# Performance work log

Hardware: AMD Instinct MI355X
Metric: run time of the kernel (lower is better)

## Reference

```python
import jax, jax.numpy as jnp
import numpy as np

# (l, C_l, C_l_TP, C_l_angular) per non-empty l-block of the filter type
FILTER_REPS = [(0, 144, 144, 1), (1, 272, 272, 1), (2, 208, 208, 1), (3, 80, 80, 1), (4, 16, 16, 1)]
FILTER_C = 720      # sum of C_l
FILTER_DIM = 2704   # sum of C_l*(2l+1)
ANG_DIM = 25        # sum of C_l_angular*(2l+1)
DIM_OUT = 52
DIM_IN = 52
Q_OUT, Q_IN, NUM_P = 16, 16, 125
SCALAR_BASIS = 12


def setup_inputs() -> dict:
    key = jax.random.key(0)
    k1, k2, k3, k4, k5 = jax.random.split(key, 5)
    N = Q_OUT * Q_IN * NUM_P
    scalar_kernel_tensor = jax.random.normal(k1, (Q_OUT, Q_IN, NUM_P, SCALAR_BASIS), dtype=jnp.float32)
    angular_kernel_tensor = jax.random.normal(k2, (N, ANG_DIM), dtype=jnp.float32)
    weights = jax.random.normal(k3, (SCALAR_BASIS, FILTER_C), dtype=jnp.float32)
    # TP mixing matrix is a constant sparse buffer (Wigner-3j based); model as sparsified dense
    dense = jax.random.normal(k4, (DIM_OUT * DIM_IN, FILTER_DIM), dtype=jnp.float32)
    mask = jax.random.uniform(k5, (DIM_OUT * DIM_IN, FILTER_DIM)) < 0.05
    TP_mixing = dense * mask.astype(jnp.float32)
    return {"scalar_kernel_tensor": scalar_kernel_tensor,
            "angular_kernel_tensor": angular_kernel_tensor,
            "weights": weights,
            "TP_mixing": TP_mixing}


def mul_scalar_angular(sc, ang):
    # sc: (N, FILTER_C), ang: (N, ANG_DIM) -> (N, FILTER_DIM)
    N = sc.shape[0]
    outs = []
    s = 0
    a = 0
    for (l, C_l, C_l_TP, C_l_ang) in FILTER_REPS:
        m = 2 * l + 1
        dim_ang = C_l_ang * m
        x = (sc[:, s:s + C_l].reshape(N, C_l_ang, C_l_TP, 1)
             * ang[:, a:a + dim_ang].reshape(N, C_l_ang, 1, m))
        outs.append(x.reshape(N, C_l * m))
        s += C_l
        a += dim_ang
    return jnp.concatenate(outs, axis=-1)


def reference(scalar_kernel_tensor, angular_kernel_tensor, weights, TP_mixing):
    N = Q_OUT * Q_IN * NUM_P
    sk = scalar_kernel_tensor.reshape(N, SCALAR_BASIS)
    # combine scalar basis with weights: (N, FILTER_C)
    sc = jnp.einsum('ns,sc->nc', sk, weights / jnp.sqrt(jnp.float32(SCALAR_BASIS)))
    # ragged segment-wise broadcast multiply: (N, FILTER_DIM)
    filt = mul_scalar_angular(sc, angular_kernel_tensor)
    # kernel = (TP_mixing @ filt.T).T == filt @ TP_mixing.T : (N, DIM_OUT*DIM_IN)
    k = filt @ TP_mixing.T
    return k.reshape(Q_OUT, Q_IN, NUM_P, DIM_OUT, DIM_IN)
```

## Files before the change

kernel.cpp:

```cpp
#include <hip/hip_runtime.h>
#include <hip/hip_bf16.h>

#define N_ROWS 32000
#define SB     12
#define FC     720
#define FD     2704
#define OCOLS  2704
#define OPAD   2816
#define ANGD   25
#define PDIM   300
#define KST    320
#define NT     5

typedef __attribute__((ext_vector_type(8))) short bf16x8;
typedef __attribute__((ext_vector_type(4))) float f32x4;

__device__ __forceinline__ void gload16(const void* g, void* l) {
    __builtin_amdgcn_global_load_lds(
        (const __attribute__((address_space(1))) void*)g,
        (__attribute__((address_space(3))) void*)l, 16, 0, 0);
}

__global__ __launch_bounds__(320) void build_V(
    const float* __restrict__ TP,
    const float* __restrict__ W,
    __hip_bfloat16* __restrict__ V)
{
    const int o   = blockIdx.x;
    const int tid = threadIdx.x;
    __shared__ float s_tp[FD];
    __shared__ float s_w[SB * FC];

    const float inv = 0.28867513459481288f;
    for (int i = tid; i < SB * FC; i += 320) s_w[i] = W[i] * inv;
    if (o < OCOLS) {
        for (int i = tid; i < FD; i += 320) s_tp[i] = TP[(size_t)o * FD + i];
    } else {
        for (int i = tid; i < FD; i += 320) s_tp[i] = 0.f;
    }
    __syncthreads();

    const int p = tid;
    float acc = 0.f;
    if (p < PDIM) {
        const int s     = p / ANGD;
        const int alpha = p - s * ANGD;
        int m, off, sco, al, Cl;
        if (alpha < 1)       { m = 1; off = 0;    sco = 0;   al = 0;  Cl = 144; }
        else if (alpha < 4)  { m = 3; off = 144;  sco = 144; al = 1;  Cl = 272; }
        else if (alpha < 9)  { m = 5; off = 960;  sco = 416; al = 4;  Cl = 208; }
        else if (alpha < 16) { m = 7; off = 2000; sco = 624; al = 9;  Cl = 80;  }
        else                 { m = 9; off = 2560; sco = 704; al = 16; Cl = 16;  }
        const int j = alpha - al;
        const float* tp = s_tp + off + j;
        const float* ww = s_w + s * FC + sco;
        float a0 = 0.f, a1 = 0.f, a2 = 0.f, a3 = 0.f;
        for (int c = 0; c < Cl; c += 4) {
            a0 += tp[(c + 0) * m] * ww[c + 0];
            a1 += tp[(c + 1) * m] * ww[c + 1];
            a2 += tp[(c + 2) * m] * ww[c + 2];
            a3 += tp[(c + 3) * m] * ww[c + 3];
        }
        acc = (a0 + a1) + (a2 + a3);
    }
    if (p < KST) V[(size_t)o * KST + p] = __float2bfloat16(acc);
}

__global__ void build_X(const float* __restrict__ sk,
                        const float* __restrict__ ang,
                        __hip_bfloat16* __restrict__ X)
{
    const int idx = blockIdx.x * 256 + threadIdx.x;
    if (idx >= N_ROWS * (KST / 8)) return;
    const int n  = idx / (KST / 8);
    const int p0 = (idx - n * (KST / 8)) * 8;
    const float* skn  = sk  + (size_t)n * SB;
    const float* angn = ang + (size_t)n * ANGD;
    alignas(16) __hip_bfloat16 tmp[8];
    #pragma unroll
    for (int u = 0; u < 8; ++u) {
        const int p = p0 + u;
        float v = 0.f;
        if (p < PDIM) {
            const int s = p / ANGD;
            const int a = p - s * ANGD;
            v = skn[s] * angn[a];
        }
        tmp[u] = __float2bfloat16(v);
    }
    *(bf16x8*)(X + (size_t)n * KST + p0) = *(const bf16x8*)tmp;
}

__global__ __launch_bounds__(512, 4) void gemm_bt(
    const __hip_bfloat16* __restrict__ A,
    const __hip_bfloat16* __restrict__ B,
    float* __restrict__ C)
{
    __shared__ __align__(1024) char lds[65536];
    char* const bufA = lds;
    char* const bufB = lds + 32768;
    float* const s_c = (float*)lds;

    const int tid  = threadIdx.x;
    const int wave = tid >> 6;
    const int lane = tid & 63;

    const int bn = blockIdx.x;
    const int bm = blockIdx.y;
    const size_t arow0 = (size_t)bm * 128;
    const size_t brow0 = (size_t)bn * 128;

    const int wr = wave >> 2;
    const int wc = wave & 3;

    const int lrow  = lane >> 3;
    const int lslot = ((lane & 7) ^ (lrow & 7)) << 4;

    auto STAGE = [&](const char* gbase, size_t growbase, int t, char* lbase) {
        const char* g0 = gbase + (growbase + (size_t)(wave * 8 + lrow)) * (KST * 2)
                               + (size_t)t * 128 + lslot;
        gload16(g0,                          lbase + wave * 1024);
        gload16(g0 + (size_t)64 * (KST * 2), lbase + 8192 + wave * 1024);
    };

    const int rl   = lane & 15;
    const int koct = lane >> 4;
    const int sK0 = ((0 * 4 + koct) ^ (lane & 7)) << 4;
    const int sK1 = ((1 * 4 + koct) ^ (lane & 7)) << 4;

    STAGE((const char*)A, arow0, 0, bufA + 0);
    STAGE((const char*)B, brow0, 0, bufB + 0);
    STAGE((const char*)A, arow0, 1, bufA + 16384);
    STAGE((const char*)B, brow0, 1, bufB + 16384);
    asm volatile("s_waitcnt vmcnt(4)" ::: "memory");
    __builtin_amdgcn_s_barrier();

    f32x4 acc[4][2] = {};

    for (int t = 0; t < NT; ++t) {
        char* const aC = bufA + (t & 1) * 16384;
        char* const bC = bufB + (t & 1) * 16384;

        bf16x8 af[4][2], bfr[2][2];
        #pragma unroll
        for (int m = 0; m < 4; ++m) {
            const int r = wr * 64 + m * 16 + rl;
            af[m][0] = *(const bf16x8*)(aC + r * 128 + sK0);
            af[m][1] = *(const bf16x8*)(aC + r * 128 + sK1);
        }
        #pragma unroll
        for (int n = 0; n < 2; ++n) {
            const int r = wc * 32 + n * 16 + rl;
            bfr[n][0] = *(const bf16x8*)(bC + r * 128 + sK0);
            bfr[n][1] = *(const bf16x8*)(bC + r * 128 + sK1);
        }
        asm volatile("s_waitcnt lgkmcnt(0)" ::: "memory");
        __builtin_amdgcn_sched_barrier(0);
        __builtin_amdgcn_s_barrier();

        if (t + 2 < NT) {
            STAGE((const char*)A, arow0, t + 2, aC);
            STAGE((const char*)B, brow0, t + 2, bC);
        }

        __builtin_amdgcn_s_setprio(1);
        #pragma unroll
        for (int ks = 0; ks < 2; ++ks)
            #pragma unroll
            for (int m = 0; m < 4; ++m)
                #pragma unroll
                for (int n = 0; n < 2; ++n)
                    acc[m][n] = __builtin_amdgcn_mfma_f32_16x16x32_bf16(
                        bfr[n][ks], af[m][ks], acc[m][n], 0, 0, 0);
        __builtin_amdgcn_s_setprio(0);
        __builtin_amdgcn_sched_barrier(0);

        if (t < NT - 2)       asm volatile("s_waitcnt vmcnt(4)" ::: "memory");
        else if (t == NT - 2) asm volatile("s_waitcnt vmcnt(0)" ::: "memory");
        if (t < NT - 1) __builtin_amdgcn_s_barrier();
    }

    #pragma unroll
    for (int h = 0; h < 2; ++h) {
        __syncthreads();
        if (wr == h) {
            #pragma unroll
            for (int m = 0; m < 4; ++m) {
                const int row_l = m * 16 + rl;
                #pragma unroll
                for (int n = 0; n < 2; ++n) {
                    const int col = wc * 32 + n * 16 + koct * 4;
                    *(f32x4*)&s_c[row_l * 132 + col] = acc[m][n];
                }
            }
        }
        __syncthreads();
        #pragma unroll
        for (int rr = 0; rr < 4; ++rr) {
            const int idx  = rr * 512 + tid;
            const int row  = idx >> 5;
            const int g4   = (idx & 31) * 4;
            if ((int)brow0 + g4 < OCOLS) {
                const f32x4 v = *(const f32x4*)&s_c[row * 132 + g4];
                __builtin_nontemporal_store(v,
                    (f32x4*)(C + (size_t)(arow0 + h * 64 + row) * OCOLS + brow0 + g4));
            }
        }
    }
}

extern "C" void kernel_launch(void* const* d_in, const int* in_sizes, int n_in,
                              void* d_out, int out_size, void* d_ws, size_t ws_size,
                              hipStream_t stream)
{
    const float* sk  = (const float*)d_in[0];
    const float* ang = (const float*)d_in[1];
    const float* W   = (const float*)d_in[2];
    const float* TP  = (const float*)d_in[3];
    float* out = (float*)d_out;

    __hip_bfloat16* X  = (__hip_bfloat16*)d_ws;
    __hip_bfloat16* Vb = X + (size_t)N_ROWS * KST;

    build_V<<<OPAD, 320, 0, stream>>>(TP, W, Vb);
    build_X<<<(N_ROWS * (KST / 8) + 255) / 256, 256, 0, stream>>>(sk, ang, X);

    dim3 grid(OPAD / 128, N_ROWS / 128);
    gemm_bt<<<grid, 512, 0, stream>>>(X, Vb, out);
}
```

Before: 156.9 us.

## Load GEMM B operand straight to registers and merge the two prep kernels

The GEMM no longer stages the B tile (V) through LDS. Each wave loads its B fragments directly from global memory into double-buffered registers one k-step ahead, while A keeps its LDS double buffer. This cuts LDS per block from 64KB to about 34KB, which can allow more resident blocks per CU, and it reorganises the vmcnt waits around the new load order. The separate build_V and build_X launches are also merged into one prep kernel, keyed on block index, to save a launch. The risk is redundant global reads of B across waves and more register pressure.

```diff
diff --git a/kernel.cpp b/kernel.cpp
--- a/kernel.cpp
+++ b/kernel.cpp
@@ -21,74 +21,74 @@
         (__attribute__((address_space(3))) void*)l, 16, 0, 0);
 }
 
-__global__ __launch_bounds__(320) void build_V(
+__global__ __launch_bounds__(320) void prep(
     const float* __restrict__ TP,
     const float* __restrict__ W,
-    __hip_bfloat16* __restrict__ V)
+    const float* __restrict__ sk,
+    const float* __restrict__ ang,
+    __hip_bfloat16* __restrict__ V,
+    __hip_bfloat16* __restrict__ X)
 {
-    const int o   = blockIdx.x;
     const int tid = threadIdx.x;
-    __shared__ float s_tp[FD];
-    __shared__ float s_w[SB * FC];
-
-    const float inv = 0.28867513459481288f;
-    for (int i = tid; i < SB * FC; i += 320) s_w[i] = W[i] * inv;
-    if (o < OCOLS) {
-        for (int i = tid; i < FD; i += 320) s_tp[i] = TP[(size_t)o * FD + i];
+    if (blockIdx.x < OPAD) {
+        const int o = blockIdx.x;
+        __shared__ float s_tp[FD];
+        __shared__ float s_w[SB * FC];
+
+        const float inv = 0.28867513459481288f;
+        for (int i = tid; i < SB * FC; i += 320) s_w[i] = W[i] * inv;
+        if (o < OCOLS) {
+            for (int i = tid; i < FD; i += 320) s_tp[i] = TP[(size_t)o * FD + i];
+        } else {
+            for (int i = tid; i < FD; i += 320) s_tp[i] = 0.f;
+        }
+        __syncthreads();
+
+        const int p = tid;
+        float acc = 0.f;
+        if (p < PDIM) {
+            const int s     = p / ANGD;
+            const int alpha = p - s * ANGD;
+            int m, off, sco, al, Cl;
+            if (alpha < 1)       { m = 1; off = 0;    sco = 0;   al = 0;  Cl = 144; }
+            else if (alpha < 4)  { m = 3; off = 144;  sco = 144; al = 1;  Cl = 272; }
+            else if (alpha < 9)  { m = 5; off = 960;  sco = 416; al = 4;  Cl = 208; }
+            else if (alpha < 16) { m = 7; off = 2000; sco = 624; al = 9;  Cl = 80;  }
+            else                 { m = 9; off = 2560; sco = 704; al = 16; Cl = 16;  }
+            const int j = alpha - al;
+            const float* tp = s_tp + off + j;
+            const float* ww = s_w + s * FC + sco;
+            float a0 = 0.f, a1 = 0.f, a2 = 0.f, a3 = 0.f;
+            for (int c = 0; c < Cl; c += 4) {
+                a0 += tp[(c + 0) * m] * ww[c + 0];
+                a1 += tp[(c + 1) * m] * ww[c + 1];
+                a2 += tp[(c + 2) * m] * ww[c + 2];
+                a3 += tp[(c + 3) * m] * ww[c + 3];
+            }
+            acc = (a0 + a1) + (a2 + a3);
+        }
+        if (p < KST) V[(size_t)o * KST + p] = __float2bfloat16(acc);
     } else {
-        for (int i = tid; i < FD; i += 320) s_tp[i] = 0.f;
+        const int idx = (blockIdx.x - OPAD) * 320 + tid;
+        if (idx >= N_ROWS * (KST / 8)) return;
+        const int n  = idx / (KST / 8);
+        const int p0 = (idx - n * (KST / 8)) * 8;
+        const float* skn  = sk  + (size_t)n * SB;
+        const float* angn = ang + (size_t)n * ANGD;
+        alignas(16) __hip_bfloat16 tmp[8];
+        #pragma unroll
+        for (int u = 0; u < 8; ++u) {
+            const int p = p0 + u;
+            float v = 0.f;
+            if (p < PDIM) {
+                const int s = p / ANGD;
+                const int a = p - s * ANGD;
+                v = skn[s] * angn[a];
+            }
+            tmp[u] = __float2bfloat16(v);
+        }
+        *(bf16x8*)(X + (size_t)n * KST + p0) = *(const bf16x8*)tmp;
     }
-    __syncthreads();
-
-    const int p = tid;
-    float acc = 0.f;
-    if (p < PDIM) {
-        const int s     = p / ANGD;
-        const int alpha = p - s * ANGD;
-        int m, off, sco, al, Cl;
-        if (alpha < 1)       { m = 1; off = 0;    sco = 0;   al = 0;  Cl = 144; }
-        else if (alpha < 4)  { m = 3; off = 144;  sco = 144; al = 1;  Cl = 272; }
-        else if (alpha < 9)  { m = 5; off = 960;  sco = 416; al = 4;  Cl = 208; }
-        else if (alpha < 16) { m = 7; off = 2000; sco = 624; al = 9;  Cl = 80;  }
-        else                 { m = 9; off = 2560; sco = 704; al = 16; Cl = 16;  }
-        const int j = alpha - al;
-        const float* tp = s_tp + off + j;
-        const float* ww = s_w + s * FC + sco;
-        float a0 = 0.f, a1 = 0.f, a2 = 0.f, a3 = 0.f;
-        for (int c = 0; c < Cl; c += 4) {
-            a0 += tp[(c + 0) * m] * ww[c + 0];
-            a1 += tp[(c + 1) * m] * ww[c + 1];
-            a2 += tp[(c + 2) * m] * ww[c + 2];
-            a3 += tp[(c + 3) * m] * ww[c + 3];
-        }
-        acc = (a0 + a1) + (a2 + a3);
-    }
-    if (p < KST) V[(size_t)o * KST + p] = __float2bfloat16(acc);
-}
-
-__global__ void build_X(const float* __restrict__ sk,
-                        const float* __restrict__ ang,
-                        __hip_bfloat16* __restrict__ X)
-{
-    const int idx = blockIdx.x * 256 + threadIdx.x;
-    if (idx >= N_ROWS * (KST / 8)) return;
-    const int n  = idx / (KST / 8);
-    const int p0 = (idx - n * (KST / 8)) * 8;
-    const float* skn  = sk  + (size_t)n * SB;
-    const float* angn = ang + (size_t)n * ANGD;
-    alignas(16) __hip_bfloat16 tmp[8];
-    #pragma unroll
-    for (int u = 0; u < 8; ++u) {
-        const int p = p0 + u;
-        float v = 0.f;
-        if (p < PDIM) {
-            const int s = p / ANGD;
-            const int a = p - s * ANGD;
-            v = skn[s] * angn[a];
-        }
-        tmp[u] = __float2bfloat16(v);
-    }
-    *(bf16x8*)(X + (size_t)n * KST + p0) = *(const bf16x8*)tmp;
 }
 
 __global__ __launch_bounds__(512, 4) void gemm_bt(
@@ -96,9 +96,8 @@
     const __hip_bfloat16* __restrict__ B,
     float* __restrict__ C)
 {
-    __shared__ __align__(1024) char lds[65536];
+    __shared__ __align__(1024) char lds[34816];
     char* const bufA = lds;
-    char* const bufB = lds + 32768;
     float* const s_c = (float*)lds;
 
     const int tid  = threadIdx.x;
@@ -115,10 +114,10 @@
 
     const int lrow  = lane >> 3;
     const int lslot = ((lane & 7) ^ (lrow & 7)) << 4;
-
-    auto STAGE = [&](const char* gbase, size_t growbase, int t, char* lbase) {
-        const char* g0 = gbase + (growbase + (size_t)(wave * 8 + lrow)) * (KST * 2)
-                               + (size_t)t * 128 + lslot;
+    auto STAGE_A = [&](int t, char* lbase) {
+        const char* g0 = (const char*)A
+            + (arow0 + (size_t)(wave * 8 + lrow)) * (KST * 2)
+            + (size_t)t * 128 + lslot;
         gload16(g0,                          lbase + wave * 1024);
         gload16(g0 + (size_t)64 * (KST * 2), lbase + 8192 + wave * 1024);
     };
@@ -128,40 +127,44 @@
     const int sK0 = ((0 * 4 + koct) ^ (lane & 7)) << 4;
     const int sK1 = ((1 * 4 + koct) ^ (lane & 7)) << 4;
 
-    STAGE((const char*)A, arow0, 0, bufA + 0);
-    STAGE((const char*)B, brow0, 0, bufB + 0);
-    STAGE((const char*)A, arow0, 1, bufA + 16384);
-    STAGE((const char*)B, brow0, 1, bufB + 16384);
-    asm volatile("s_waitcnt vmcnt(4)" ::: "memory");
+    const char* const Bb = (const char*)B;
+    const size_t boff0 = (brow0 + (size_t)(wc * 32 + 0 * 16 + rl)) * (KST * 2) + koct * 16;
+    const size_t boff1 = (brow0 + (size_t)(wc * 32 + 1 * 16 + rl)) * (KST * 2) + koct * 16;
+
+    bf16x8 bfr[2][2][2];
+    auto LOADB = [&](int t, int slot) {
+        bfr[slot][0][0] = *(const bf16x8*)(Bb + boff0 + t * 128 + 0);
+        bfr[slot][0][1] = *(const bf16x8*)(Bb + boff0 + t * 128 + 64);
+        bfr[slot][1][0] = *(const bf16x8*)(Bb + boff1 + t * 128 + 0);
+        bfr[slot][1][1] = *(const bf16x8*)(Bb + boff1 + t * 128 + 64);
+    };
+
+    STAGE_A(0, bufA + 0);
+    STAGE_A(1, bufA + 16384);
+    LOADB(0, 0);
+    asm volatile("s_waitcnt vmcnt(0)" ::: "memory");
     __builtin_amdgcn_s_barrier();
 
     f32x4 acc[4][2] = {};
 
+    #pragma unroll
     for (int t = 0; t < NT; ++t) {
         char* const aC = bufA + (t & 1) * 16384;
-        char* const bC = bufB + (t & 1) * 16384;
-
-        bf16x8 af[4][2], bfr[2][2];
+
+        if (t + 1 < NT) LOADB(t + 1, (t + 1) & 1);
+
+        bf16x8 af[4][2];
         #pragma unroll
         for (int m = 0; m < 4; ++m) {
             const int r = wr * 64 + m * 16 + rl;
             af[m][0] = *(const bf16x8*)(aC + r * 128 + sK0);
             af[m][1] = *(const bf16x8*)(aC + r * 128 + sK1);
         }
-        #pragma unroll
-        for (int n = 0; n < 2; ++n) {
-            const int r = wc * 32 + n * 16 + rl;
-            bfr[n][0] = *(const bf16x8*)(bC + r * 128 + sK0);
-            bfr[n][1] = *(const bf16x8*)(bC + r * 128 + sK1);
-        }
         asm volatile("s_waitcnt lgkmcnt(0)" ::: "memory");
         __builtin_amdgcn_sched_barrier(0);
         __builtin_amdgcn_s_barrier();
 
-        if (t + 2 < NT) {
-            STAGE((const char*)A, arow0, t + 2, aC);
-            STAGE((const char*)B, brow0, t + 2, bC);
-        }
+        if (t + 2 < NT) STAGE_A(t + 2, aC);
 
         __builtin_amdgcn_s_setprio(1);
         #pragma unroll
@@ -171,11 +174,11 @@
                 #pragma unroll
                 for (int n = 0; n < 2; ++n)
                     acc[m][n] = __builtin_amdgcn_mfma_f32_16x16x32_bf16(
-                        bfr[n][ks], af[m][ks], acc[m][n], 0, 0, 0);
+                        bfr[t & 1][n][ks], af[m][ks], acc[m][n], 0, 0, 0);
         __builtin_amdgcn_s_setprio(0);
         __builtin_amdgcn_sched_barrier(0);
 
-        if (t < NT - 2)       asm volatile("s_waitcnt vmcnt(4)" ::: "memory");
+        if (t < NT - 2)       asm volatile("s_waitcnt vmcnt(2)" ::: "memory");
         else if (t == NT - 2) asm volatile("s_waitcnt vmcnt(0)" ::: "memory");
         if (t < NT - 1) __builtin_amdgcn_s_barrier();
     }
@@ -222,8 +225,7 @@
     __hip_bfloat16* X  = (__hip_bfloat16*)d_ws;
     __hip_bfloat16* Vb = X + (size_t)N_ROWS * KST;
 
-    build_V<<<OPAD, 320, 0, stream>>>(TP, W, Vb);
-    build_X<<<(N_ROWS * (KST / 8) + 255) / 256, 256, 0, stream>>>(sk, ang, X);
+    prep<<<OPAD + 4000, 320, 0, stream>>>(TP, W, sk, ang, Vb, X);
 
     dim3 grid(OPAD / 128, N_ROWS / 128);
     gemm_bt<<<grid, 512, 0, stream>>>(X, Vb, out);
```

Result: slower. 206.8 us (+31.8%).

## Shrink GEMM tile to 128x64 with 256 threads and K-step of 32

Applied to the files above, without the earlier changes.

Reworks the GEMM so each block computes a 128x64 output tile with 4 waves, and halves the K-slice per pipeline stage, which doubles the number of K iterations. The LDS footprint drops from 64KB to 24KB, with a new swizzle pattern for the 64-byte rows. The aim is higher occupancy and more blocks to spread the store-bound output across CUs. In exchange, B-operand reuse per block drops, A is loaded twice as often across the grid, and there are more barriers per unit of work.

```diff
diff --git a/kernel.cpp b/kernel.cpp
--- a/kernel.cpp
+++ b/kernel.cpp
@@ -10,7 +10,7 @@
 #define ANGD   25
 #define PDIM   300
 #define KST    320
-#define NT     5
+#define NT     10
 
 typedef __attribute__((ext_vector_type(8))) short bf16x8;
 typedef __attribute__((ext_vector_type(4))) float f32x4;
@@ -91,14 +91,14 @@
     *(bf16x8*)(X + (size_t)n * KST + p0) = *(const bf16x8*)tmp;
 }
 
-__global__ __launch_bounds__(512, 4) void gemm_bt(
+__global__ __launch_bounds__(256, 4) void gemm_bt(
     const __hip_bfloat16* __restrict__ A,
     const __hip_bfloat16* __restrict__ B,
     float* __restrict__ C)
 {
-    __shared__ __align__(1024) char lds[65536];
+    __shared__ __align__(1024) char lds[24576];
     char* const bufA = lds;
-    char* const bufB = lds + 32768;
+    char* const bufB = lds + 16384;
     float* const s_c = (float*)lds;
 
     const int tid  = threadIdx.x;
@@ -108,74 +108,71 @@
     const int bn = blockIdx.x;
     const int bm = blockIdx.y;
     const size_t arow0 = (size_t)bm * 128;
-    const size_t brow0 = (size_t)bn * 128;
-
-    const int wr = wave >> 2;
-    const int wc = wave & 3;
-
-    const int lrow  = lane >> 3;
-    const int lslot = ((lane & 7) ^ (lrow & 7)) << 4;
-
-    auto STAGE = [&](const char* gbase, size_t growbase, int t, char* lbase) {
-        const char* g0 = gbase + (growbase + (size_t)(wave * 8 + lrow)) * (KST * 2)
-                               + (size_t)t * 128 + lslot;
-        gload16(g0,                          lbase + wave * 1024);
-        gload16(g0 + (size_t)64 * (KST * 2), lbase + 8192 + wave * 1024);
+    const size_t brow0 = (size_t)bn * 64;
+
+    const int wr = wave >> 1;
+    const int wc = wave & 1;
+
+    const int lrow2 = lane >> 2;
+    const int sslot = (((lane & 3) ^ (lrow2 & 3) ^ ((lane >> 4) & 3))) << 4;
+
+    auto STAGE = [&](int t, int half) {
+        char* const la = bufA + half * 8192;
+        char* const lb = bufB + half * 4096;
+        const char* ga = (const char*)A
+            + (arow0 + (size_t)(wave * 16 + lrow2)) * (KST * 2)
+            + (size_t)t * 64 + sslot;
+        gload16(ga,                          la + wave * 1024);
+        gload16(ga + (size_t)64 * (KST * 2), la + 4096 + wave * 1024);
+        const char* gb = (const char*)B
+            + (brow0 + (size_t)(wave * 16 + lrow2)) * (KST * 2)
+            + (size_t)t * 64 + sslot;
+        gload16(gb, lb + wave * 1024);
     };
 
     const int rl   = lane & 15;
     const int koct = lane >> 4;
-    const int sK0 = ((0 * 4 + koct) ^ (lane & 7)) << 4;
-    const int sK1 = ((1 * 4 + koct) ^ (lane & 7)) << 4;
-
-    STAGE((const char*)A, arow0, 0, bufA + 0);
-    STAGE((const char*)B, brow0, 0, bufB + 0);
-    STAGE((const char*)A, arow0, 1, bufA + 16384);
-    STAGE((const char*)B, brow0, 1, bufB + 16384);
-    asm volatile("s_waitcnt vmcnt(4)" ::: "memory");
+    const int rslot = ((koct ^ (rl & 3) ^ ((rl >> 2) & 3))) << 4;
+
+    STAGE(0, 0);
+    STAGE(1, 1);
+    asm volatile("s_waitcnt vmcnt(3)" ::: "memory");
     __builtin_amdgcn_s_barrier();
 
     f32x4 acc[4][2] = {};
 
     for (int t = 0; t < NT; ++t) {
-        char* const aC = bufA + (t & 1) * 16384;
-        char* const bC = bufB + (t & 1) * 16384;
-
-        bf16x8 af[4][2], bfr[2][2];
+        char* const aC = bufA + (t & 1) * 8192;
+        char* const bC = bufB + (t & 1) * 4096;
+
+        bf16x8 af[4], bfr[2];
         #pragma unroll
         for (int m = 0; m < 4; ++m) {
             const int r = wr * 64 + m * 16 + rl;
-            af[m][0] = *(const bf16x8*)(aC + r * 128 + sK0);
-            af[m][1] = *(const bf16x8*)(aC + r * 128 + sK1);
+            af[m] = *(const bf16x8*)(aC + r * 64 + rslot);
         }
         #pragma unroll
         for (int n = 0; n < 2; ++n) {
             const int r = wc * 32 + n * 16 + rl;
-            bfr[n][0] = *(const bf16x8*)(bC + r * 128 + sK0);
-            bfr[n][1] = *(const bf16x8*)(bC + r * 128 + sK1);
+            bfr[n] = *(const bf16x8*)(bC + r * 64 + rslot);
         }
         asm volatile("s_waitcnt lgkmcnt(0)" ::: "memory");
         __builtin_amdgcn_sched_barrier(0);
         __builtin_amdgcn_s_barrier();
 
-        if (t + 2 < NT) {
-            STAGE((const char*)A, arow0, t + 2, aC);
-            STAGE((const char*)B, brow0, t + 2, bC);
-        }
+        if (t + 2 < NT) STAGE(t + 2, t & 1);
 
         __builtin_amdgcn_s_setprio(1);
         #pragma unroll
-        for (int ks = 0; ks < 2; ++ks)
+        for (int m = 0; m < 4; ++m)
             #pragma unroll
-            for (int m = 0; m < 4; ++m)
-                #pragma unroll
-                for (int n = 0; n < 2; ++n)
-                    acc[m][n] = __builtin_amdgcn_mfma_f32_16x16x32_bf16(
-                        bfr[n][ks], af[m][ks], acc[m][n], 0, 0, 0);
+            for (int n = 0; n < 2; ++n)
+                acc[m][n] = __builtin_amdgcn_mfma_f32_16x16x32_bf16(
+                    bfr[n], af[m], acc[m][n], 0, 0, 0);
         __builtin_amdgcn_s_setprio(0);
         __builtin_amdgcn_sched_barrier(0);
 
-        if (t < NT - 2)       asm volatile("s_waitcnt vmcnt(4)" ::: "memory");
+        if (t < NT - 2)       asm volatile("s_waitcnt vmcnt(3)" ::: "memory");
         else if (t == NT - 2) asm volatile("s_waitcnt vmcnt(0)" ::: "memory");
         if (t < NT - 1) __builtin_amdgcn_s_barrier();
     }
@@ -190,18 +187,18 @@
                 #pragma unroll
                 for (int n = 0; n < 2; ++n) {
                     const int col = wc * 32 + n * 16 + koct * 4;
-                    *(f32x4*)&s_c[row_l * 132 + col] = acc[m][n];
+                    *(f32x4*)&s_c[row_l * 68 + col] = acc[m][n];
                 }
             }
         }
         __syncthreads();
         #pragma unroll
         for (int rr = 0; rr < 4; ++rr) {
-            const int idx  = rr * 512 + tid;
-            const int row  = idx >> 5;
-            const int g4   = (idx & 31) * 4;
+            const int idx = rr * 256 + tid;
+            const int row = idx >> 4;
+            const int g4  = (idx & 15) * 4;
             if ((int)brow0 + g4 < OCOLS) {
-                const f32x4 v = *(const f32x4*)&s_c[row * 132 + g4];
+                const f32x4 v = *(const f32x4*)&s_c[row * 68 + g4];
                 __builtin_nontemporal_store(v,
                     (f32x4*)(C + (size_t)(arow0 + h * 64 + row) * OCOLS + brow0 + g4));
             }
@@ -225,6 +222,6 @@
     build_V<<<OPAD, 320, 0, stream>>>(TP, W, Vb);
     build_X<<<(N_ROWS * (KST / 8) + 255) / 256, 256, 0, stream>>>(sk, ang, X);
 
-    dim3 grid(OPAD / 128, N_ROWS / 128);
-    gemm_bt<<<grid, 512, 0, stream>>>(X, Vb, out);
-}
+    dim3 grid(OPAD / 64, N_ROWS / 128);
+    gemm_bt<<<grid, 256, 0, stream>>>(X, Vb, out);
+}
```

Result: slower. 174.6 us (+11.3%).

## Compute TP-weight projection V with an MFMA GEMM over a dense expanded weight matrix

Applied to the files above, without the earlier changes.

Replaces the scalar per-block build_V reduction with a three-step path. TP_mixing is converted to bf16, an expanded sparse-structured G matrix is built from the weights and the l-block structure, and V = TP·G is computed with a bf16 MFMA GEMM. The aim is to cut the cost of the strided, serial LDS dot products in build_V. In exchange it adds two extra kernel launches and more workspace traffic. It also quantizes TP to bf16 before the reduction, which adds precision loss, and it performs many multiplies by zero in G.

```diff
diff --git a/kernel.cpp b/kernel.cpp
--- a/kernel.cpp
+++ b/kernel.cpp
@@ -11,6 +11,9 @@
 #define PDIM   300
 #define KST    320
 #define NT     5
+#define KP     2720
+#define NTV    85
+#define GPR    (KP/8)
 
 typedef __attribute__((ext_vector_type(8))) short bf16x8;
 typedef __attribute__((ext_vector_type(4))) float f32x4;
@@ -21,49 +24,60 @@
         (__attribute__((address_space(3))) void*)l, 16, 0, 0);
 }
 
-__global__ __launch_bounds__(320) void build_V(
-    const float* __restrict__ TP,
-    const float* __restrict__ W,
-    __hip_bfloat16* __restrict__ V)
-{
-    const int o   = blockIdx.x;
-    const int tid = threadIdx.x;
-    __shared__ float s_tp[FD];
-    __shared__ float s_w[SB * FC];
-
+__device__ __forceinline__ void decode_f(int f, int& c, int& j, int& a) {
+    if (f < 144)       { c = f;                         j = 0;            a = 0;  }
+    else if (f < 960)  { int t = f - 144;  c = 144 + t/3; j = t - (t/3)*3; a = 1;  }
+    else if (f < 2000) { int t = f - 960;  c = 416 + t/5; j = t - (t/5)*5; a = 4;  }
+    else if (f < 2560) { int t = f - 2000; c = 624 + t/7; j = t - (t/7)*7; a = 9;  }
+    else               { int t = f - 2560; c = 704 + t/9; j = t - (t/9)*9; a = 16; }
+}
+
+__global__ void cvt_M(const float* __restrict__ M, __hip_bfloat16* __restrict__ out)
+{
+    const int g = blockIdx.x * 256 + threadIdx.x;
+    if (g >= OPAD * GPR) return;
+    const int o = g / GPR;
+    const int k = (g - o * GPR) * 8;
+    alignas(16) __hip_bfloat16 tmp[8];
+    if (o < OCOLS && k + 8 <= FD) {
+        const float4* p = (const float4*)(M + (size_t)o * FD + k);
+        float4 x0 = p[0], x1 = p[1];
+        tmp[0] = __float2bfloat16(x0.x); tmp[1] = __float2bfloat16(x0.y);
+        tmp[2] = __float2bfloat16(x0.z); tmp[3] = __float2bfloat16(x0.w);
+        tmp[4] = __float2bfloat16(x1.x); tmp[5] = __float2bfloat16(x1.y);
+        tmp[6] = __float2bfloat16(x1.z); tmp[7] = __float2bfloat16(x1.w);
+    } else {
+        #pragma unroll
+        for (int u = 0; u < 8; ++u) {
+            float v = (o < OCOLS && k + u < FD) ? M[(size_t)o * FD + k + u] : 0.f;
+            tmp[u] = __float2bfloat16(v);
+        }
+    }
+    *(bf16x8*)(out + (size_t)o * KP + k) = *(const bf16x8*)tmp;
+}
+
+__global__ void build_G(const float* __restrict__ W, __hip_bfloat16* __restrict__ Gt)
+{
+    const int g = blockIdx.x * 256 + threadIdx.x;
+    if (g >= KST * GPR) return;
+    const int p  = g / GPR;
+    const int f0 = (g - p * GPR) * 8;
+    const int s     = p / ANGD;
+    const int alpha = p - s * ANGD;
     const float inv = 0.28867513459481288f;
-    for (int i = tid; i < SB * FC; i += 320) s_w[i] = W[i] * inv;
-    if (o < OCOLS) {
-        for (int i = tid; i < FD; i += 320) s_tp[i] = TP[(size_t)o * FD + i];
-    } else {
-        for (int i = tid; i < FD; i += 320) s_tp[i] = 0.f;
-    }
-    __syncthreads();
-
-    const int p = tid;
-    float acc = 0.f;
-    if (p < PDIM) {
-        const int s     = p / ANGD;
-        const int alpha = p - s * ANGD;
-        int m, off, sco, al, Cl;
-        if (alpha < 1)       { m = 1; off = 0;    sco = 0;   al = 0;  Cl = 144; }
-        else if (alpha < 4)  { m = 3; off = 144;  sco = 144; al = 1;  Cl = 272; }
-        else if (alpha < 9)  { m = 5; off = 960;  sco = 416; al = 4;  Cl = 208; }
-        else if (alpha < 16) { m = 7; off = 2000; sco = 624; al = 9;  Cl = 80;  }
-        else                 { m = 9; off = 2560; sco = 704; al = 16; Cl = 16;  }
-        const int j = alpha - al;
-        const float* tp = s_tp + off + j;
-        const float* ww = s_w + s * FC + sco;
-        float a0 = 0.f, a1 = 0.f, a2 = 0.f, a3 = 0.f;
-        for (int c = 0; c < Cl; c += 4) {
-            a0 += tp[(c + 0) * m] * ww[c + 0];
-            a1 += tp[(c + 1) * m] * ww[c + 1];
-            a2 += tp[(c + 2) * m] * ww[c + 2];
-            a3 += tp[(c + 3) * m] * ww[c + 3];
-        }
-        acc = (a0 + a1) + (a2 + a3);
-    }
-    if (p < KST) V[(size_t)o * KST + p] = __float2bfloat16(acc);
+    alignas(16) __hip_bfloat16 tmp[8];
+    #pragma unroll
+    for (int u = 0; u < 8; ++u) {
+        const int f = f0 + u;
+        float v = 0.f;
+        if (p < PDIM && f < FD) {
+            int c, j, a;
+            decode_f(f, c, j, a);
+            if (alpha == a + j) v = W[s * FC + c] * inv;
+        }
+        tmp[u] = __float2bfloat16(v);
+    }
+    *(bf16x8*)(Gt + (size_t)p * KP + f0) = *(const bf16x8*)tmp;
 }
 
 __global__ void build_X(const float* __restrict__ sk,
@@ -91,6 +105,109 @@
     *(bf16x8*)(X + (size_t)n * KST + p0) = *(const bf16x8*)tmp;
 }
 
+__global__ __launch_bounds__(256, 4) void gemm_V(
+    const __hip_bfloat16* __restrict__ A,
+    const __hip_bfloat16* __restrict__ B,
+    __hip_bfloat16* __restrict__ V)
+{
+    __shared__ __align__(1024) char lds[24576];
+    char* const bufA = lds;
+    char* const bufB = lds + 16384;
+
+    const int tid  = threadIdx.x;
+    const int wave = tid >> 6;
+    const int lane = tid & 63;
+
+    const int bn = blockIdx.x;
+    const int bm = blockIdx.y;
+    const size_t arow0 = (size_t)bm * 128;
+    const size_t brow0 = (size_t)bn * 64;
+
+    const int wr = wave >> 1;
+    const int wc = wave & 1;
+
+    const int lrow2 = lane >> 2;
+    const int sslot = (((lane & 3) ^ (lrow2 & 3) ^ ((lane >> 4) & 3))) << 4;
+
+    auto STAGE = [&](int t, int half) {
+        char* const la = bufA + half * 8192;
+        char* const lb = bufB + half * 4096;
+        const char* ga = (const char*)A
+            + (arow0 + (size_t)(wave * 16 + lrow2)) * (KP * 2)
+            + (size_t)t * 64 + sslot;
+        gload16(ga,                         la + wave * 1024);
+        gload16(ga + (size_t)64 * (KP * 2), la + 4096 + wave * 1024);
+        const char* gb = (const char*)B
+            + (brow0 + (size_t)(wave * 16 + lrow2)) * (KP * 2)
+            + (size_t)t * 64 + sslot;
+        gload16(gb, lb + wave * 1024);
+    };
+
+    const int rl   = lane & 15;
+    const int koct = lane >> 4;
+    const int rslot = ((koct ^ (rl & 3) ^ ((rl >> 2) & 3))) << 4;
+
+    STAGE(0, 0);
+    STAGE(1, 1);
+    asm volatile("s_waitcnt vmcnt(3)" ::: "memory");
+    __builtin_amdgcn_s_barrier();
+
+    f32x4 acc[4][2] = {};
+
+    for (int t = 0; t < NTV; ++t) {
+        char* const aC = bufA + (t & 1) * 8192;
+        char* const bC = bufB + (t & 1) * 4096;
+
+        bf16x8 af[4], bfr[2];
+        #pragma unroll
+        for (int m = 0; m < 4; ++m) {
+            const int r = wr * 64 + m * 16 + rl;
+            af[m] = *(const bf16x8*)(aC + r * 64 + rslot);
+        }
+        #pragma unroll
+        for (int n = 0; n < 2; ++n) {
+            const int r = wc * 32 + n * 16 + rl;
+            bfr[n] = *(const bf16x8*)(bC + r * 64 + rslot);
+        }
+        asm volatile("s_waitcnt lgkmcnt(0)" ::: "memory");
+        __builtin_amdgcn_sched_barrier(0);
+        __builtin_amdgcn_s_barrier();
+
+        if (t + 2 < NTV) STAGE(t + 2, t & 1);
+
+        __builtin_amdgcn_s_setprio(1);
+        #pragma unroll
+        for (int m = 0; m < 4; ++m)
+            #pragma unroll
+            for (int n = 0; n < 2; ++n)
+                acc[m][n] = __builtin_amdgcn_mfma_f32_16x16x32_bf16(
+                    bfr[n], af[m], acc[m][n], 0, 0, 0);
+        __builtin_amdgcn_s_setprio(0);
+        __builtin_amdgcn_sched_barrier(0);
+
+        if (t < NTV - 2)       asm volatile("s_waitcnt vmcnt(3)" ::: "memory");
+        else if (t == NTV - 2) asm volatile("s_waitcnt vmcnt(0)" ::: "memory");
+        if (t < NTV - 1) __builtin_amdgcn_s_barrier();
+    }
+
+    const int obase = (int)arow0 + wr * 64 + rl;
+    const int pbase = (int)brow0 + wc * 32 + koct * 4;
+    #pragma unroll
+    for (int m = 0; m < 4; ++m) {
+        const int orow = obase + m * 16;
+        #pragma unroll
+        for (int n = 0; n < 2; ++n) {
+            const int p = pbase + n * 16;
+            alignas(8) __hip_bfloat16 t4[4];
+            t4[0] = __float2bfloat16(acc[m][n][0]);
+            t4[1] = __float2bfloat16(acc[m][n][1]);
+            t4[2] = __float2bfloat16(acc[m][n][2]);
+            t4[3] = __float2bfloat16(acc[m][n][3]);
+            *(uint2*)(V + (size_t)orow * KST + p) = *(const uint2*)t4;
+        }
+    }
+}
+
 __global__ __launch_bounds__(512, 4) void gemm_bt(
     const __hip_bfloat16* __restrict__ A,
     const __hip_bfloat16* __restrict__ B,
@@ -219,11 +336,17 @@
     const float* TP  = (const float*)d_in[3];
     float* out = (float*)d_out;
 
-    __hip_bfloat16* X  = (__hip_bfloat16*)d_ws;
-    __hip_bfloat16* Vb = X + (size_t)N_ROWS * KST;
-
-    build_V<<<OPAD, 320, 0, stream>>>(TP, W, Vb);
+    __hip_bfloat16* X   = (__hip_bfloat16*)d_ws;
+    __hip_bfloat16* Vb  = X   + (size_t)N_ROWS * KST;
+    __hip_bfloat16* TPb = Vb  + (size_t)OPAD * KST;
+    __hip_bfloat16* Gt  = TPb + (size_t)OPAD * KP;
+
+    cvt_M<<<(OPAD * GPR + 255) / 256, 256, 0, stream>>>(TP, TPb);
+    build_G<<<(KST * GPR + 255) / 256, 256, 0, stream>>>(W, Gt);
     build_X<<<(N_ROWS * (KST / 8) + 255) / 256, 256, 0, stream>>>(sk, ang, X);
+
+    dim3 gridV(KST / 64, OPAD / 128);
+    gemm_V<<<gridV, 256, 0, stream>>>(TPb, Gt, Vb);
 
     dim3 grid(OPAD / 128, N_ROWS / 128);
     gemm_bt<<<grid, 512, 0, stream>>>(X, Vb, out);
```

Result: faster. 141.5 us (-9.8%).
